# Kernel tuning notes

Measured on AMD Instinct MI355X. Metric: run time of the kernel, lower is better.

## Reference

```python
import jax, jax.numpy as jnp
import numpy as np
from jax import lax

T, B, S, D, V = 128, 512, 128, 128, 50257


def setup_inputs() -> dict:
    key = jax.random.key(0)
    ks = jax.random.split(key, 6)
    words = jax.random.randint(ks[0], (T, B), 0, V, dtype=jnp.int64)
    masks = jnp.ones((T, B), dtype=jnp.float32)
    tparams = jax.random.normal(ks[1], (S, S), dtype=jnp.float32)
    tag_embed = jax.random.normal(ks[2], (S, D), dtype=jnp.float32)
    word_embed = jax.random.normal(ks[3], (V, D), dtype=jnp.float32)
    transform = jax.random.normal(ks[4], (D, D), dtype=jnp.float32) * 0.05 + jnp.eye(D, dtype=jnp.float32)
    correction = jax.random.normal(ks[5], (S, V), dtype=jnp.float32) * 0.05
    return {"words": words, "masks": masks, "tparams": tparams,
            "tag_embed": tag_embed, "word_embed": word_embed,
            "transform": transform, "correction": correction}


def reference(words, masks, tparams, tag_embed, word_embed, transform, correction):
    num_state = tparams.shape[0]
    # update_emission (unsupervised mode): project word embeddings, score against tags,
    # add correction, log_softmax over the vocab dimension (dim=0 of (V,S)).
    word_emb = word_embed @ transform                      # (V, D)
    log_emission = jax.nn.log_softmax(word_emb @ tag_embed.T + correction.T, axis=0)  # (V, S)
    # _calc_logA: log-normalized transition matrix (rows = source state)
    logA = jax.nn.log_softmax(tparams, axis=1)             # (S, S)
    # uniform log prior pi = log(1/S)
    log_pi = jnp.full((num_state,), jnp.log(1.0 / num_state), dtype=log_emission.dtype)

    em = log_emission[words]                               # (T, B, S) gathered densities

    alpha0 = log_pi[None, :] + em[0]                       # (B, S)

    def step(alpha, inp):
        dens, m = inp                                      # (B,S), (B,)
        # _forward_cell: logsumexp over previous state of alpha + logA + density
        new = jax.nn.logsumexp(alpha[:, :, None] + logA[None, :, :] + dens[:, None, :], axis=1)
        m = m[:, None]
        alpha = m * new + (1.0 - m) * alpha
        return alpha, None

    alpha, _ = lax.scan(step, alpha0, (em[1:], masks[1:]))
    objective = jnp.sum(jax.nn.logsumexp(alpha, axis=1))
    return -objective
```

## Files before the change

kernel.cpp:

```cpp
#include <hip/hip_runtime.h>
#include <math.h>

#define T_ 128
#define B_ 512
#define S_ 128
#define D_ 128
#define V_ 50257

#define K2_VT 64
#define K2_NB ((V_ + K2_VT - 1) / K2_VT)

__global__ __launch_bounds__(128) void k1_fused(const float* __restrict__ transform,
                                                const float* __restrict__ tag_embed,
                                                const float* __restrict__ tparams,
                                                float* __restrict__ M2,
                                                float* __restrict__ A) {
  int tid = threadIdx.x;
  int bid = blockIdx.x;
  if (bid < 128) {
    __shared__ float te[128][129];
    for (int r = 0; r < 128; ++r) te[r][tid] = tag_embed[r * 128 + tid];
    __syncthreads();
    int k = bid;
    float acc = 0.f;
    #pragma unroll 8
    for (int d = 0; d < 128; ++d) acc += transform[k * 128 + d] * te[tid][d];
    M2[k * 128 + tid] = acc;
  } else {
    if (tid < 64) {
      int i = bid - 128;
      int l = tid;
      float x0 = tparams[i * 128 + l];
      float x1 = tparams[i * 128 + 64 + l];
      float m = fmaxf(x0, x1);
      #pragma unroll
      for (int off = 32; off; off >>= 1) m = fmaxf(m, __shfl_xor(m, off));
      float e0 = __expf(x0 - m), e1 = __expf(x1 - m);
      float s = e0 + e1;
      #pragma unroll
      for (int off = 32; off; off >>= 1) s += __shfl_xor(s, off);
      float inv = 1.f / s;
      A[i * 128 + l]      = e0 * inv;
      A[i * 128 + 64 + l] = e1 * inv;
    }
  }
}

#define K2STEP(COMP, KK) { \
  float4 mv = *(const float4*)&m2t[(KK)][4 * sc]; \
  acc[0][0] += wr[0].COMP * mv.x; acc[0][1] += wr[0].COMP * mv.y; acc[0][2] += wr[0].COMP * mv.z; acc[0][3] += wr[0].COMP * mv.w; \
  acc[1][0] += wr[1].COMP * mv.x; acc[1][1] += wr[1].COMP * mv.y; acc[1][2] += wr[1].COMP * mv.z; acc[1][3] += wr[1].COMP * mv.w; \
  acc[2][0] += wr[2].COMP * mv.x; acc[2][1] += wr[2].COMP * mv.y; acc[2][2] += wr[2].COMP * mv.z; acc[2][3] += wr[2].COMP * mv.w; \
  acc[3][0] += wr[3].COMP * mv.x; acc[3][1] += wr[3].COMP * mv.y; acc[3][2] += wr[3].COMP * mv.z; acc[3][3] += wr[3].COMP * mv.w; \
  acc[4][0] += wr[4].COMP * mv.x; acc[4][1] += wr[4].COMP * mv.y; acc[4][2] += wr[4].COMP * mv.z; acc[4][3] += wr[4].COMP * mv.w; \
  acc[5][0] += wr[5].COMP * mv.x; acc[5][1] += wr[5].COMP * mv.y; acc[5][2] += wr[5].COMP * mv.z; acc[5][3] += wr[5].COMP * mv.w; \
  acc[6][0] += wr[6].COMP * mv.x; acc[6][1] += wr[6].COMP * mv.y; acc[6][2] += wr[6].COMP * mv.z; acc[6][3] += wr[6].COMP * mv.w; \
  acc[7][0] += wr[7].COMP * mv.x; acc[7][1] += wr[7].COMP * mv.y; acc[7][2] += wr[7].COMP * mv.z; acc[7][3] += wr[7].COMP * mv.w; }

__global__ __launch_bounds__(256, 4) void k2_logits(const float* __restrict__ we,
                                                 const float* __restrict__ M2,
                                                 const float* __restrict__ corr,
                                                 float* __restrict__ logits,
                                                 float* __restrict__ pmaxb,
                                                 float* __restrict__ psumb) {
  int tid = threadIdx.x;
  int sc = tid & 31;
  int vg = tid >> 5;
  unsigned v0 = (unsigned)blockIdx.x * K2_VT;
  __shared__ float m2t[64][128];

  unsigned vrow[8];
  #pragma unroll
  for (int u = 0; u < 8; ++u) {
    unsigned v = v0 + 8 * vg + u;
    vrow[u] = (v < V_ ? v : (V_ - 1)) * 128u;
  }

  float acc[8][4];
  #pragma unroll
  for (int u = 0; u < 8; ++u)
    #pragma unroll
    for (int e = 0; e < 4; ++e) acc[u][e] = 0.f;

  #pragma unroll
  for (int c = 0; c < 2; ++c) {
    __syncthreads();
    #pragma unroll
    for (int it = 0; it < 8; ++it) {
      int idx = it * 256 + tid;
      int kr = idx >> 5;
      int scol = (idx & 31) * 4;
      *(float4*)&m2t[kr][scol] = *(const float4*)&M2[(c * 64 + kr) * 128 + scol];
    }
    __syncthreads();
    #pragma unroll 4
    for (int kc = 0; kc < 64; kc += 4) {
      float4 wr[8];
      #pragma unroll
      for (int u = 0; u < 8; ++u)
        wr[u] = *(const float4*)&we[vrow[u] + (unsigned)(c * 64 + kc)];
      K2STEP(x, kc + 0)
      K2STEP(y, kc + 1)
      K2STEP(z, kc + 2)
      K2STEP(w, kc + 3)
    }
  }

  float lm[4], ls[4], Lst[8][4];
  #pragma unroll
  for (int e = 0; e < 4; ++e) { lm[e] = -INFINITY; ls[e] = 0.f; }
  long vbase = (long)v0 + 8 * vg;
  #pragma unroll
  for (int e = 0; e < 4; ++e) {
    long rbase = (long)(4 * sc + e) * V_ + vbase;
    #pragma unroll
    for (int u = 0; u < 8; ++u) {
      if (vbase + u < V_) {
        float L = acc[u][e] + corr[rbase + u];
        Lst[u][e] = L;
        float nm = fmaxf(lm[e], L);
        ls[e] = ls[e] * __expf(lm[e] - nm) + __expf(L - nm);
        lm[e] = nm;
      }
    }
  }
  #pragma unroll
  for (int u = 0; u < 8; ++u) {
    long v = vbase + u;
    if (v < V_) {
      float4 st = make_float4(Lst[u][0], Lst[u][1], Lst[u][2], Lst[u][3]);
      *(float4*)&logits[v * 128 + 4 * sc] = st;
    }
  }

  __syncthreads();
  float* pmx = (float*)m2t;
  float* psm = pmx + 8 * 128;
  #pragma unroll
  for (int e = 0; e < 4; ++e) {
    pmx[vg * 128 + 4 * sc + e] = lm[e];
    psm[vg * 128 + 4 * sc + e] = ls[e];
  }
  __syncthreads();
  if (tid < 128) {
    int s = tid;
    float m = -INFINITY, sum = 0.f;
    #pragma unroll
    for (int g = 0; g < 8; ++g) {
      float pm = pmx[g * 128 + s];
      if (pm > -1e30f) {
        float ps = psm[g * 128 + s];
        float nm = fmaxf(m, pm);
        sum = sum * __expf(m - nm) + ps * __expf(pm - nm);
        m = nm;
      }
    }
    pmaxb[blockIdx.x * 128 + s] = m;
    psumb[blockIdx.x * 128 + s] = sum;
  }
}

__global__ __launch_bounds__(256) void k3_c(const float* __restrict__ pmaxb,
                                            const float* __restrict__ psumb,
                                            float* __restrict__ C) {
  int s = blockIdx.x;
  int t = threadIdx.x;
  float m = -INFINITY, sum = 0.f;
  #pragma unroll
  for (int q = 0; q < 4; ++q) {
    int b = t + q * 256;
    if (b < K2_NB) {
      float pm = pmaxb[b * 128 + s];
      if (pm > -1e30f) {
        float ps = psumb[b * 128 + s];
        float nm = fmaxf(m, pm);
        sum = sum * __expf(m - nm) + ps * __expf(pm - nm);
        m = nm;
      }
    }
  }
  #pragma unroll
  for (int off = 32; off; off >>= 1) {
    float om = __shfl_xor(m, off);
    float os = __shfl_xor(sum, off);
    float nm = fmaxf(m, om);
    sum = sum * __expf(m - nm) + os * __expf(om - nm);
    m = nm;
  }
  __shared__ float wm[4], wsv[4];
  int lane = t & 63, wv = t >> 6;
  if (lane == 0) { wm[wv] = m; wsv[wv] = sum; }
  __syncthreads();
  if (t == 0) {
    float M = fmaxf(fmaxf(wm[0], wm[1]), fmaxf(wm[2], wm[3]));
    float S = wsv[0] * __expf(wm[0] - M) + wsv[1] * __expf(wm[1] - M)
            + wsv[2] * __expf(wm[2] - M) + wsv[3] * __expf(wm[3] - M);
    C[s] = M + __logf(S);
  }
}

__global__ __launch_bounds__(512, 4) void k4_rec(const int* __restrict__ words,
                                              const float* __restrict__ masks,
                                              const float* __restrict__ A,
                                              const float* __restrict__ C,
                                              const float* __restrict__ logits,
                                              float* __restrict__ bv) {
  const float kB = 70.70101247f;
  int tid = threadIdx.x;
  int j = tid & 127;
  int h = tid >> 7;
  int b = blockIdx.x;
  int lane = tid & 63, w = tid >> 6;
  __shared__ __align__(16) float els[128];
  __shared__ float part[4][128];
  __shared__ __align__(16) float pmax4[4];
  __shared__ float wred[2];
  __shared__ int   wbuf[128];
  __shared__ float mbuf[128];
  if (tid < 128) {
    wbuf[j] = words[j * B_ + b];
    mbuf[j] = masks[j * B_ + b];
  }
  float Ac[32];
  #pragma unroll
  for (int k = 0; k < 32; ++k) Ac[k] = A[(h * 32 + k) * 128 + j];
  __syncthreads();

  float a = 0.f, S = 0.f, em_cur = 0.f, Lnext = 0.f, Cj = 0.f, a0 = 0.f;
  if (tid < 128) {
    __builtin_amdgcn_s_setprio(1);
    Cj = C[j];
    a0 = -4.852030263919617f + logits[(unsigned)(wbuf[0] * 128 + j)] - Cj;
    float wm = a0;
    #pragma unroll
    for (int off = 32; off; off >>= 1) wm = fmaxf(wm, __shfl_xor(wm, off));
    if (lane == 0) wred[w] = wm;
  }
  __syncthreads();
  if (tid < 128) {
    float M0 = fmaxf(wred[0], wred[1]);
    a = __expf(a0 - M0);
    S = M0;
    els[j] = a;
    float L1 = logits[(unsigned)(wbuf[1] * 128 + j)];
    Lnext    = logits[(unsigned)(wbuf[2] * 128 + j)];
    em_cur = __expf(L1 - Cj + kB);
  }
  __syncthreads();

  for (int t = 1; t < T_; ++t) {
    float4 e0 = ((const float4*)els)[h * 8 + 0];
    float4 e1 = ((const float4*)els)[h * 8 + 1];
    float4 e2 = ((const float4*)els)[h * 8 + 2];
    float4 e3 = ((const float4*)els)[h * 8 + 3];
    float4 e4 = ((const float4*)els)[h * 8 + 4];
    float4 e5 = ((const float4*)els)[h * 8 + 5];
    float4 e6 = ((const float4*)els)[h * 8 + 6];
    float4 e7 = ((const float4*)els)[h * 8 + 7];
    float p0 = e0.x * Ac[0]  + e0.y * Ac[1]  + e0.z * Ac[2]  + e0.w * Ac[3]
             + e1.x * Ac[4]  + e1.y * Ac[5]  + e1.z * Ac[6]  + e1.w * Ac[7];
    float p1 = e2.x * Ac[8]  + e2.y * Ac[9]  + e2.z * Ac[10] + e2.w * Ac[11]
             + e3.x * Ac[12] + e3.y * Ac[13] + e3.z * Ac[14] + e3.w * Ac[15];
    float p2 = e4.x * Ac[16] + e4.y * Ac[17] + e4.z * Ac[18] + e4.w * Ac[19]
             + e5.x * Ac[20] + e5.y * Ac[21] + e5.z * Ac[22] + e5.w * Ac[23];
    float p3 = e6.x * Ac[24] + e6.y * Ac[25] + e6.z * Ac[26] + e6.w * Ac[27]
             + e7.x * Ac[28] + e7.y * Ac[29] + e7.z * Ac[30] + e7.w * Ac[31];
    part[h][j] = (p0 + p1) + (p2 + p3);
    if (j == 0) {
      float4 ma = make_float4(fmaxf(e0.x, e1.x), fmaxf(e0.y, e1.y), fmaxf(e0.z, e1.z), fmaxf(e0.w, e1.w));
      float4 mb = make_float4(fmaxf(e2.x, e3.x), fmaxf(e2.y, e3.y), fmaxf(e2.z, e3.z), fmaxf(e2.w, e3.w));
      float4 mc = make_float4(fmaxf(e4.x, e5.x), fmaxf(e4.y, e5.y), fmaxf(e4.z, e5.z), fmaxf(e4.w, e5.w));
      float4 md = make_float4(fmaxf(e6.x, e7.x), fmaxf(e6.y, e7.y), fmaxf(e6.z, e7.z), fmaxf(e6.w, e7.w));
      float4 m1 = make_float4(fmaxf(ma.x, mb.x), fmaxf(ma.y, mb.y), fmaxf(ma.z, mb.z), fmaxf(ma.w, mb.w));
      float4 m2 = make_float4(fmaxf(mc.x, md.x), fmaxf(mc.y, md.y), fmaxf(mc.z, md.z), fmaxf(mc.w, md.w));
      float mx = fmaxf(fmaxf(fmaxf(m1.x, m1.y), fmaxf(m1.z, m1.w)),
                       fmaxf(fmaxf(m2.x, m2.y), fmaxf(m2.z, m2.w)));
      pmax4[h] = mx;
    }
    float em_next = 0.f, Lf = 0.f;
    if (tid < 128) {
      if (t + 2 < T_) Lf = logits[(unsigned)(wbuf[t + 2] * 128 + j)];
      em_next = __expf(Lnext - Cj + kB);
    }
    __syncthreads();
    if (tid < 128) {
      __builtin_amdgcn_s_setprio(2);
      float4 pm4 = *(const float4*)pmax4;
      float Mst = fmaxf(fmaxf(pm4.x, pm4.y), fmaxf(pm4.z, pm4.w));
      float invM = 1.f / Mst;
      float P = (part[0][j] + part[1][j]) + (part[2][j] + part[3][j]);
      float nv   = (P * invM) * em_cur;
      float oldq = (a * invM) * 0x1p102f;
      float mm = mbuf[t];
      a = mm * nv + (1.f - mm) * oldq;
      els[j] = a;
      S += __logf(Mst) - kB;
      em_cur = em_next;
      Lnext = Lf;
      __builtin_amdgcn_s_setprio(1);
    }
    __syncthreads();
  }

  if (tid < 128) {
    float ss = a;
    #pragma unroll
    for (int off = 32; off; off >>= 1) ss += __shfl_xor(ss, off);
    if (lane == 0) wred[w] = ss;
  }
  __syncthreads();
  if (tid == 0) bv[b] = S + __logf(wred[0] + wred[1]);
}

__global__ __launch_bounds__(256) void k5_sum(const float* __restrict__ bv,
                                              float* __restrict__ out) {
  int t = threadIdx.x;
  float s = bv[t] + bv[t + 256];
  #pragma unroll
  for (int off = 32; off; off >>= 1) s += __shfl_xor(s, off);
  __shared__ float wsm[4];
  if ((t & 63) == 0) wsm[t >> 6] = s;
  __syncthreads();
  if (t == 0) out[0] = -(wsm[0] + wsm[1] + wsm[2] + wsm[3]);
}

extern "C" void kernel_launch(void* const* d_in, const int* in_sizes, int n_in,
                              void* d_out, int out_size, void* d_ws, size_t ws_size,
                              hipStream_t stream) {
  const int*   words      = (const int*)d_in[0];
  const float* masks      = (const float*)d_in[1];
  const float* tparams    = (const float*)d_in[2];
  const float* tag_embed  = (const float*)d_in[3];
  const float* word_embed = (const float*)d_in[4];
  const float* transform  = (const float*)d_in[5];
  const float* correction = (const float*)d_in[6];

  float* ws     = (float*)d_ws;
  float* M2     = ws;
  float* A      = ws + 16384;
  float* C      = ws + 32768;
  float* bv     = ws + 32896;
  float* pmaxb  = ws + 33408;
  float* psumb  = ws + 134016;
  float* logits = ws + 234624;

  hipLaunchKernelGGL(k1_fused, dim3(256),    dim3(128), 0, stream, transform, tag_embed, tparams, M2, A);
  hipLaunchKernelGGL(k2_logits,dim3(K2_NB),  dim3(256), 0, stream, word_embed, M2, correction, logits, pmaxb, psumb);
  hipLaunchKernelGGL(k3_c,     dim3(S_),     dim3(256), 0, stream, pmaxb, psumb, C);
  hipLaunchKernelGGL(k4_rec,   dim3(512),    dim3(512), 0, stream, words, masks, A, C, logits, bv);
  hipLaunchKernelGGL(k5_sum,   dim3(1),      dim3(256), 0, stream, bv, (float*)d_out);
}
```

Before: 170.3 us.

## Offload emission prefetch to idle wave and compute row max via shuffles

Moves the per-step emission gather and exp off the critical threads into the h==2 waves, which write it to shared memory each step. The max of alpha is now computed by the updating threads with a wave shuffle reduction into a double-buffered shared array, replacing the serial max over els done by the j==0 threads. The aim is to shorten the serial per-step critical path of the recurrence. In exchange it adds shuffle work on the critical wave and couples correctness to the double-buffer parity indexing.

```diff
diff --git a/kernel.cpp b/kernel.cpp
--- a/kernel.cpp
+++ b/kernel.cpp
@@ -213,8 +213,9 @@
   int lane = tid & 63, w = tid >> 6;
   __shared__ __align__(16) float els[128];
   __shared__ float part[4][128];
-  __shared__ __align__(16) float pmax4[4];
+  __shared__ float wredM[2][2];
   __shared__ float wred[2];
+  __shared__ float em_lds[128];
   __shared__ int   wbuf[128];
   __shared__ float mbuf[128];
   if (tid < 128) {
@@ -226,15 +227,21 @@
   for (int k = 0; k < 32; ++k) Ac[k] = A[(h * 32 + k) * 128 + j];
   __syncthreads();
 
-  float a = 0.f, S = 0.f, em_cur = 0.f, Lnext = 0.f, Cj = 0.f, a0 = 0.f;
-  if (tid < 128) {
-    __builtin_amdgcn_s_setprio(1);
+  if (h == 0 || h == 2) __builtin_amdgcn_s_setprio(1);
+
+  float a = 0.f, S = 0.f, Cj = 0.f, a0 = 0.f;
+  float Lc = 0.f, Cj2 = 0.f;
+  if (tid < 128) {
     Cj = C[j];
     a0 = -4.852030263919617f + logits[(unsigned)(wbuf[0] * 128 + j)] - Cj;
     float wm = a0;
     #pragma unroll
     for (int off = 32; off; off >>= 1) wm = fmaxf(wm, __shfl_xor(wm, off));
     if (lane == 0) wred[w] = wm;
+  }
+  if (h == 2) {
+    Cj2 = C[j];
+    Lc = logits[(unsigned)(wbuf[1] * 128 + j)];
   }
   __syncthreads();
   if (tid < 128) {
@@ -242,13 +249,18 @@
     a = __expf(a0 - M0);
     S = M0;
     els[j] = a;
-    float L1 = logits[(unsigned)(wbuf[1] * 128 + j)];
-    Lnext    = logits[(unsigned)(wbuf[2] * 128 + j)];
-    em_cur = __expf(L1 - Cj + kB);
+    float wx = a;
+    #pragma unroll
+    for (int off = 32; off; off >>= 1) wx = fmaxf(wx, __shfl_xor(wx, off));
+    if (lane == 0) wredM[0][w] = wx;
   }
   __syncthreads();
 
   for (int t = 1; t < T_; ++t) {
+    if (h == 2) {
+      em_lds[j] = __expf(Lc - Cj2 + kB);
+      if (t + 1 < T_) Lc = logits[(unsigned)(wbuf[t + 1] * 128 + j)];
+    }
     float4 e0 = ((const float4*)els)[h * 8 + 0];
     float4 e1 = ((const float4*)els)[h * 8 + 1];
     float4 e2 = ((const float4*)els)[h * 8 + 2];
@@ -266,37 +278,23 @@
     float p3 = e6.x * Ac[24] + e6.y * Ac[25] + e6.z * Ac[26] + e6.w * Ac[27]
              + e7.x * Ac[28] + e7.y * Ac[29] + e7.z * Ac[30] + e7.w * Ac[31];
     part[h][j] = (p0 + p1) + (p2 + p3);
-    if (j == 0) {
-      float4 ma = make_float4(fmaxf(e0.x, e1.x), fmaxf(e0.y, e1.y), fmaxf(e0.z, e1.z), fmaxf(e0.w, e1.w));
-      float4 mb = make_float4(fmaxf(e2.x, e3.x), fmaxf(e2.y, e3.y), fmaxf(e2.z, e3.z), fmaxf(e2.w, e3.w));
-      float4 mc = make_float4(fmaxf(e4.x, e5.x), fmaxf(e4.y, e5.y), fmaxf(e4.z, e5.z), fmaxf(e4.w, e5.w));
-      float4 md = make_float4(fmaxf(e6.x, e7.x), fmaxf(e6.y, e7.y), fmaxf(e6.z, e7.z), fmaxf(e6.w, e7.w));
-      float4 m1 = make_float4(fmaxf(ma.x, mb.x), fmaxf(ma.y, mb.y), fmaxf(ma.z, mb.z), fmaxf(ma.w, mb.w));
-      float4 m2 = make_float4(fmaxf(mc.x, md.x), fmaxf(mc.y, md.y), fmaxf(mc.z, md.z), fmaxf(mc.w, md.w));
-      float mx = fmaxf(fmaxf(fmaxf(m1.x, m1.y), fmaxf(m1.z, m1.w)),
-                       fmaxf(fmaxf(m2.x, m2.y), fmaxf(m2.z, m2.w)));
-      pmax4[h] = mx;
-    }
-    float em_next = 0.f, Lf = 0.f;
-    if (tid < 128) {
-      if (t + 2 < T_) Lf = logits[(unsigned)(wbuf[t + 2] * 128 + j)];
-      em_next = __expf(Lnext - Cj + kB);
-    }
     __syncthreads();
     if (tid < 128) {
       __builtin_amdgcn_s_setprio(2);
-      float4 pm4 = *(const float4*)pmax4;
-      float Mst = fmaxf(fmaxf(pm4.x, pm4.y), fmaxf(pm4.z, pm4.w));
+      float Mst = fmaxf(wredM[(t + 1) & 1][0], wredM[(t + 1) & 1][1]);
       float invM = 1.f / Mst;
       float P = (part[0][j] + part[1][j]) + (part[2][j] + part[3][j]);
-      float nv   = (P * invM) * em_cur;
+      float emv = em_lds[j];
+      float mm = mbuf[t];
+      float nv   = (P * invM) * emv;
       float oldq = (a * invM) * 0x1p102f;
-      float mm = mbuf[t];
       a = mm * nv + (1.f - mm) * oldq;
       els[j] = a;
       S += __logf(Mst) - kB;
-      em_cur = em_next;
-      Lnext = Lf;
+      float wx = a;
+      #pragma unroll
+      for (int off = 32; off; off >>= 1) wx = fmaxf(wx, __shfl_xor(wx, off));
+      if (lane == 0) wredM[t & 1][w] = wx;
       __builtin_amdgcn_s_setprio(1);
     }
     __syncthreads();
```

Result: slower. 185.8 us (+9.1%).
